# Kernel tuning notes

Measured on AMD Instinct MI355X. Metric: run time of the kernel, lower is better.

Reference implementation:

```python
import jax, jax.numpy as jnp
import numpy as np

DIM = 2048
HEADS = 16
DIM_HEAD = 128
DIM_INNER = HEADS * DIM_HEAD
BATCH = 2
SEQ = 2048
EPS = 1e-12  # F.normalize default eps


def l2norm(t, axis=-1):
    # matches F.normalize(t, dim=axis, p=2): t / max(||t||, eps)
    n = jnp.sqrt(jnp.sum(t * t, axis=axis, keepdims=True))
    return t / jnp.maximum(n, EPS)


def setup_inputs() -> dict:
    key = jax.random.key(0)
    ks = jax.random.split(key, 5)
    x = jax.random.normal(ks[0], (BATCH, SEQ, DIM), dtype=jnp.float32)
    # NormLinear weights (torch Linear layout: [out, in]); parametrization
    # l2-normalizes rows (dim=-1) for q/k/v and columns (dim=0) for to_out.
    Wq = jax.random.normal(ks[1], (DIM_INNER, DIM), dtype=jnp.float32) / np.sqrt(DIM)
    Wk = jax.random.normal(ks[2], (DIM_INNER, DIM), dtype=jnp.float32) / np.sqrt(DIM)
    Wv = jax.random.normal(ks[3], (DIM_INNER, DIM), dtype=jnp.float32) / np.sqrt(DIM)
    Wout = jax.random.normal(ks[4], (DIM, DIM_INNER), dtype=jnp.float32) / np.sqrt(DIM_INNER)
    # Scale(dim_inner, init=1.0, scale=dim**-1): param = ones * dim**-1,
    # forward_scale = init/scale = dim, so qk_scale() starts at 1.0
    qk_scale = jnp.ones((DIM_INNER,), dtype=jnp.float32) / DIM
    return {"x": x, "Wq": Wq, "Wk": Wk, "Wv": Wv, "Wout": Wout, "qk_scale": qk_scale}


def reference(x, Wq, Wk, Wv, Wout, qk_scale):
    b, n, _ = x.shape
    # NormLinear: x @ l2norm(W, rows).T  (scale = groups**-1 = 1)
    q = jnp.einsum('bnd,ed->bne', x, l2norm(Wq, axis=-1))
    k = jnp.einsum('bnd,ed->bne', x, l2norm(Wk, axis=-1))
    v = jnp.einsum('bnd,ed->bne', x, l2norm(Wv, axis=-1))
    # split heads: b n (h d) -> b h n d
    split = lambda t: t.reshape(b, n, HEADS, DIM_HEAD).transpose(0, 2, 1, 3)
    q, k, v = split(q), split(k), split(v)
    # per-head l2norm of q and k over head dim
    q = l2norm(q, axis=-1)
    k = l2norm(k, axis=-1)
    # learned qk scale: (h d) -> h 1 d, effective = param * forward_scale(=DIM)
    q = q * (qk_scale * DIM).reshape(HEADS, 1, DIM_HEAD)
    # causal SDPA with scale = sqrt(dim_head) (unit-norm q,k in nGPT)
    attn_scale = DIM_HEAD ** 0.5
    scores = jnp.einsum('bhid,bhjd->bhij', q, k) * attn_scale
    causal = jnp.tril(jnp.ones((n, n), dtype=bool))
    scores = jnp.where(causal, scores, jnp.finfo(scores.dtype).min)
    attn = jax.nn.softmax(scores, axis=-1)
    out = jnp.einsum('bhij,bhjd->bhid', attn, v)
    # merge heads: b h n d -> b n (h d)
    out = out.transpose(0, 2, 1, 3).reshape(b, n, DIM_INNER)
    # to_out: NormLinear with norm over dim=0 of weight [DIM, DIM_INNER]
    out = jnp.einsum('bne,de->bnd', out, l2norm(Wout, axis=0))
    return out
```

## Files before the change

kernel.cpp:

```cpp
#include <hip/hip_runtime.h>


typedef __bf16 bf16x8 __attribute__((ext_vector_type(8)));
typedef float f32x4 __attribute__((ext_vector_type(4)));

__device__ __forceinline__ unsigned short f2bf(float f) {
  unsigned int u = __float_as_uint(f);
  u = u + 0x7FFFu + ((u >> 16) & 1u);
  return (unsigned short)(u >> 16);
}

__device__ __forceinline__ void async16(const void* g, void* l) {
  __builtin_amdgcn_global_load_lds(
      (const __attribute__((address_space(1))) unsigned int*)g,
      (__attribute__((address_space(3))) unsigned int*)l, 16, 0, 0);
}

#define QFOLD (2048.0f * 11.313708498984761f * 1.4426950408889634f)


__global__ __launch_bounds__(256) void prep_w_rows(
    const float* __restrict__ Wq, const float* __restrict__ Wk,
    const float* __restrict__ Wv, ushort* __restrict__ oq,
    ushort* __restrict__ ok_, ushort* __restrict__ ov) {
  const int row = blockIdx.x;
  const float* W = (blockIdx.y == 0) ? Wq : (blockIdx.y == 1) ? Wk : Wv;
  ushort* O = (blockIdx.y == 0) ? oq : (blockIdx.y == 1) ? ok_ : ov;
  const int t = threadIdx.x;
  const float4* Wr = (const float4*)(W + (size_t)row * 2048);
  float4 v0 = Wr[t];
  float4 v1 = Wr[t + 256];
  float ss = v0.x * v0.x + v0.y * v0.y + v0.z * v0.z + v0.w * v0.w +
             v1.x * v1.x + v1.y * v1.y + v1.z * v1.z + v1.w * v1.w;
  ss += __shfl_xor(ss, 1);  ss += __shfl_xor(ss, 2);
  ss += __shfl_xor(ss, 4);  ss += __shfl_xor(ss, 8);
  ss += __shfl_xor(ss, 16); ss += __shfl_xor(ss, 32);
  __shared__ float red[4];
  if ((t & 63) == 0) red[t >> 6] = ss;
  __syncthreads();
  float tot = red[0] + red[1] + red[2] + red[3];
  float sc = 1.0f / fmaxf(sqrtf(tot), 1e-12f);
  ushort4 o0, o1;
  o0.x = f2bf(v0.x * sc); o0.y = f2bf(v0.y * sc);
  o0.z = f2bf(v0.z * sc); o0.w = f2bf(v0.w * sc);
  o1.x = f2bf(v1.x * sc); o1.y = f2bf(v1.y * sc);
  o1.z = f2bf(v1.z * sc); o1.w = f2bf(v1.w * sc);
  *(ushort4*)(O + (size_t)row * 2048 + t * 4) = o0;
  *(ushort4*)(O + (size_t)row * 2048 + 1024 + t * 4) = o1;
}

__global__ __launch_bounds__(256) void wout_colss(const float* __restrict__ W,
                                                  float* __restrict__ colss) {
  const int e = blockIdx.x * 256 + threadIdx.x;
  const int d0 = blockIdx.y * 128;
  float ss = 0.f;
  #pragma unroll 8
  for (int i = 0; i < 128; ++i) {
    float v = W[(size_t)(d0 + i) * 2048 + e];
    ss += v * v;
  }
  atomicAdd(colss + e, ss);
}

__global__ __launch_bounds__(256) void wout_norm(const float* __restrict__ W,
                                                 const float* __restrict__ colss,
                                                 ushort* __restrict__ O) {
  const int idx = (blockIdx.x * 256 + threadIdx.x) * 4;
  float4 v = *(const float4*)(W + idx);
  float4 c = *(const float4*)(colss + (idx & 2047));
  ushort4 o;
  o.x = f2bf(v.x / fmaxf(sqrtf(c.x), 1e-12f));
  o.y = f2bf(v.y / fmaxf(sqrtf(c.y), 1e-12f));
  o.z = f2bf(v.z / fmaxf(sqrtf(c.z), 1e-12f));
  o.w = f2bf(v.w / fmaxf(sqrtf(c.w), 1e-12f));
  *(ushort4*)(O + idx) = o;
}

__global__ __launch_bounds__(256) void convert_x(const float* __restrict__ X,
                                                 ushort* __restrict__ O) {
  const int idx = (blockIdx.x * 256 + threadIdx.x) * 4;
  float4 v = *(const float4*)(X + idx);
  ushort4 o;
  o.x = f2bf(v.x); o.y = f2bf(v.y); o.z = f2bf(v.z); o.w = f2bf(v.w);
  *(ushort4*)(O + idx) = o;
}

__global__ __launch_bounds__(64) void qk_mhead(const float* __restrict__ qks,
                                               float* __restrict__ mh) {
  const int h = blockIdx.x, l = threadIdx.x;
  float m = fmaxf(fabsf(qks[h * 128 + l]), fabsf(qks[h * 128 + 64 + l]));
  m = fmaxf(m, __shfl_xor(m, 1));  m = fmaxf(m, __shfl_xor(m, 2));
  m = fmaxf(m, __shfl_xor(m, 4));  m = fmaxf(m, __shfl_xor(m, 8));
  m = fmaxf(m, __shfl_xor(m, 16)); m = fmaxf(m, __shfl_xor(m, 32));
  if (l == 0) mh[h] = m * QFOLD;
}


#define LDSBUF 49152
#define ABYTES 32768

__device__ __forceinline__ void mainloop_256x128(
    const ushort* __restrict__ A, const ushort* __restrict__ Bw,
    int m0, int n0, char* lds, f32x4 acc[4][4], int t) {
  const int l = t & 63, w = t >> 6;
  const int wm = w & 3, wn = w >> 2;
  const int l15 = l & 15, l4 = l >> 4;

  const int lc = (t & 7) ^ ((t >> 3) & 7);
  const ushort* srcA = A + (size_t)m0 * 2048 + (t >> 3) * 2048 + lc * 8;
  const ushort* srcB = Bw + (size_t)n0 * 2048 + (t >> 3) * 2048 + lc * 8;
  char* dstA = lds + t * 16;
  char* dstB = lds + ABYTES + t * 16;

  const int rdA = (wm * 64 + l15) * 128;
  const int rdB = ABYTES + (wn * 64 + l15) * 128;
  const int cb0 = ((l4 ^ (l15 & 7)) * 16);
  const int cb1 = (((4 + l4) ^ (l15 & 7)) * 16);

  auto stageA = [&](int s, int k0, int o) {
    async16(srcA + (size_t)o * 131072 + k0, dstA + s * LDSBUF + o * 8192);
  };
  auto stageB = [&](int s, int k0, int o) {
    async16(srcB + (size_t)o * 131072 + k0, dstB + s * LDSBUF + o * 8192);
  };

  #pragma unroll
  for (int i = 0; i < 4; ++i)
    #pragma unroll
    for (int j = 0; j < 4; ++j) acc[i][j] = (f32x4){0.f, 0.f, 0.f, 0.f};

  stageA(0, 0, 0); stageA(0, 0, 1); stageA(0, 0, 2); stageA(0, 0, 3);
  stageB(0, 0, 0); stageB(0, 0, 1);
  stageA(1, 64, 0); stageA(1, 64, 1); stageA(1, 64, 2); stageA(1, 64, 3);
  stageB(1, 64, 0); stageB(1, 64, 1);
  asm volatile("s_waitcnt vmcnt(6)" ::: "memory");
  __builtin_amdgcn_s_barrier();

  auto tile = [&](int s, int s2, int k2, bool pf) {
    const char* Ab = lds + s * LDSBUF;
    bf16x8 af[4][2], bg[4][2];
    #pragma unroll
    for (int fm = 0; fm < 4; ++fm) {
      af[fm][0] = *(const bf16x8*)(Ab + rdA + fm * 2048 + cb0);
      af[fm][1] = *(const bf16x8*)(Ab + rdA + fm * 2048 + cb1);
    }
    #pragma unroll
    for (int fn = 0; fn < 2; ++fn) {
      bg[fn][0] = *(const bf16x8*)(Ab + rdB + fn * 2048 + cb0);
      bg[fn][1] = *(const bf16x8*)(Ab + rdB + fn * 2048 + cb1);
    }
    if (pf) { stageA(s2, k2, 0); stageA(s2, k2, 1); stageA(s2, k2, 2); }
    __builtin_amdgcn_s_setprio(1);
    #pragma unroll
    for (int ks = 0; ks < 2; ++ks)
      #pragma unroll
      for (int fm = 0; fm < 4; ++fm)
        #pragma unroll
        for (int fn = 0; fn < 2; ++fn)
          acc[fm][fn] = __builtin_amdgcn_mfma_f32_16x16x32_bf16(
              af[fm][ks], bg[fn][ks], acc[fm][fn], 0, 0, 0);
    __builtin_amdgcn_s_setprio(0);
    #pragma unroll
    for (int fn = 2; fn < 4; ++fn) {
      bg[fn][0] = *(const bf16x8*)(Ab + rdB + fn * 2048 + cb0);
      bg[fn][1] = *(const bf16x8*)(Ab + rdB + fn * 2048 + cb1);
    }
    if (pf) { stageA(s2, k2, 3); stageB(s2, k2, 0); stageB(s2, k2, 1); }
    __builtin_amdgcn_s_setprio(1);
    #pragma unroll
    for (int ks = 0; ks < 2; ++ks)
      #pragma unroll
      for (int fm = 0; fm < 4; ++fm)
        #pragma unroll
        for (int fn = 2; fn < 4; ++fn)
          acc[fm][fn] = __builtin_amdgcn_mfma_f32_16x16x32_bf16(
              af[fm][ks], bg[fn][ks], acc[fm][fn], 0, 0, 0);
    __builtin_amdgcn_s_setprio(0);
  };

  #pragma unroll 1
  for (int kt = 0; kt < 30; kt += 3) {
    tile(0, 2, (kt + 2) * 64, true);
    asm volatile("s_waitcnt vmcnt(6)" ::: "memory");
    __builtin_amdgcn_s_barrier();
    tile(1, 0, (kt + 3) * 64, true);
    asm volatile("s_waitcnt vmcnt(6)" ::: "memory");
    __builtin_amdgcn_s_barrier();
    tile(2, 1, (kt + 4) * 64, true);
    asm volatile("s_waitcnt vmcnt(6)" ::: "memory");
    __builtin_amdgcn_s_barrier();
  }
  tile(0, 0, 0, false);
  asm volatile("s_waitcnt vmcnt(0)" ::: "memory");
  __builtin_amdgcn_s_barrier();
  tile(1, 0, 0, false);
}

__global__ __launch_bounds__(512, 2) void gemm_qkv(
    const ushort* __restrict__ X, const ushort* __restrict__ Wq,
    const ushort* __restrict__ Wk, const ushort* __restrict__ Wv,
    const float* __restrict__ qks, ushort* __restrict__ qn,
    ushort* __restrict__ kn, ushort* __restrict__ vt) {
  __shared__ __align__(16) char lds[3 * LDSBUF];
  __shared__ float partials[2][256];
  const int z = blockIdx.z;
  const ushort* Bw = (z == 0) ? Wq : (z == 1) ? Wk : Wv;
  const int n0 = blockIdx.x * 128;
  const int m0 = blockIdx.y * 256;
  const int t = threadIdx.x;
  const int l = t & 63, w = t >> 6;
  const int wm = w & 3, wn = w >> 2;
  const int l15 = l & 15, l4 = l >> 4;

  f32x4 acc[4][4];
  mainloop_256x128(X, Bw, m0, n0, lds, acc, t);

  const int h = blockIdx.x;
  if (z == 2) {
    const int bb = m0 >> 11, nb = m0 & 2047;
    #pragma unroll
    for (int fm = 0; fm < 4; ++fm) {
      int nn = nb + wm * 64 + fm * 16 + l4 * 4;
      #pragma unroll
      for (int fn = 0; fn < 4; ++fn) {
        int d = wn * 64 + fn * 16 + l15;
        ushort4 p;
        p.x = f2bf(acc[fm][fn][0]); p.y = f2bf(acc[fm][fn][1]);
        p.z = f2bf(acc[fm][fn][2]); p.w = f2bf(acc[fm][fn][3]);
        *(ushort4*)(vt + (size_t)((bb * 16 + h) * 128 + d) * 2048 + nn) = p;
      }
    }
  } else {
    #pragma unroll
    for (int fm = 0; fm < 4; ++fm)
      #pragma unroll
      for (int r = 0; r < 4; ++r) {
        float s = 0.f;
        #pragma unroll
        for (int fn = 0; fn < 4; ++fn) {
          float v = acc[fm][fn][r];
          s += v * v;
        }
        s += __shfl_xor(s, 1); s += __shfl_xor(s, 2);
        s += __shfl_xor(s, 4); s += __shfl_xor(s, 8);
        if (l15 == 0) partials[wn][wm * 64 + fm * 16 + l4 * 4 + r] = s;
      }
    __syncthreads();
    float cs[4];
    #pragma unroll
    for (int fn = 0; fn < 4; ++fn)
      cs[fn] = (z == 0) ? qks[n0 + wn * 64 + fn * 16 + l15] * QFOLD : 1.0f;
    ushort* O = (z == 0) ? qn : kn;
    #pragma unroll
    for (int fm = 0; fm < 4; ++fm)
      #pragma unroll
      for (int r = 0; r < 4; ++r) {
        int i = wm * 64 + fm * 16 + l4 * 4 + r;
        float tot = partials[0][i] + partials[1][i];
        float sc = 1.0f / fmaxf(sqrtf(tot), 1e-12f);
        #pragma unroll
        for (int fn = 0; fn < 4; ++fn)
          O[(size_t)(m0 + i) * 2048 + n0 + wn * 64 + fn * 16 + l15] =
              f2bf(acc[fm][fn][r] * sc * cs[fn]);
      }
  }
}

__global__ __launch_bounds__(256, 3) void attn_kernel(
    const ushort* __restrict__ qn, const ushort* __restrict__ kn,
    const ushort* __restrict__ vt, const float* __restrict__ mhead,
    ushort* __restrict__ ao) {
  const int hb = blockIdx.x;
  const int b = hb >> 4, h = hb & 15;
  const int qt = 31 - blockIdx.y;
  const int i0 = qt * 64;
  const int t = threadIdx.x, w = t >> 6, l = t & 63;
  const int l15 = l & 15, l4 = l >> 4;

  __shared__ __align__(16) ushort Ks[64 * 136];
  __shared__ __align__(16) ushort Vts[128 * 72];
  __shared__ __align__(16) ushort Ps[64 * 72];

  bf16x8 qf[4];
  #pragma unroll
  for (int ks = 0; ks < 4; ++ks)
    qf[ks] = *(const bf16x8*)(qn +
        (size_t)(b * 2048 + i0 + w * 16 + l15) * 2048 +
        h * 128 + ks * 32 + l4 * 8);

  f32x4 Oa[8];
  #pragma unroll
  for (int fd = 0; fd < 8; ++fd) Oa[fd] = (f32x4){0.f, 0.f, 0.f, 0.f};
  f32x4 Ol = (f32x4){0.f, 0.f, 0.f, 0.f};

  const float mh = mhead[h];
  const __bf16 one = (__bf16)1.0f;
  const bf16x8 ones = {one, one, one, one, one, one, one, one};

  const ushort* kbase = kn + (size_t)(b * 2048) * 2048 + h * 128;
  const ushort* vbase = vt + (size_t)((b * 16 + h) * 128) * 2048;

  for (int jt = 0; jt <= qt; ++jt) {
    const int j0 = jt * 64;
    __syncthreads();
    #pragma unroll
    for (int pass = 0; pass < 5; ++pass) {
      int c = pass * 256 + t;
      if (c < 1088) {
        int r = c / 17, dc = c - r * 17;
        int dcc = (dc == 16) ? 0 : dc;
        async16(kbase + (size_t)(j0 + r) * 2048 + dcc * 8, (char*)Ks + c * 16);
      }
    }
    #pragma unroll
    for (int pass = 0; pass < 5; ++pass) {
      int c = pass * 256 + t;
      if (c < 1152) {
        int r = c / 9, jc = c - r * 9;
        int jcc = (jc == 8) ? 0 : jc;
        async16(vbase + (size_t)r * 2048 + j0 + jcc * 8, (char*)Vts + c * 16);
      }
    }
    __syncthreads();

    f32x4 Sa[4];
    #pragma unroll
    for (int fj = 0; fj < 4; ++fj) {
      f32x4 s0 = (f32x4){0.f, 0.f, 0.f, 0.f};
      #pragma unroll
      for (int ks = 0; ks < 4; ++ks) {
        bf16x8 kf = *(const bf16x8*)&Ks[(fj * 16 + l15) * 136 + ks * 32 + l4 * 8];
        s0 = __builtin_amdgcn_mfma_f32_16x16x32_bf16(qf[ks], kf, s0, 0, 0, 0);
      }
      Sa[fj] = s0;
    }

    if (jt == qt) {
      #pragma unroll
      for (int fj = 0; fj < 4; ++fj)
        #pragma unroll
        for (int r = 0; r < 4; ++r) {
          int jg = fj * 16 + l15;
          int ig = w * 16 + l4 * 4 + r;
          if (jg > ig) Sa[fj][r] = -1e30f;
        }
    }

    #pragma unroll
    for (int fj = 0; fj < 4; ++fj)
      #pragma unroll
      for (int r = 0; r < 4; ++r)
        Ps[(w * 16 + l4 * 4 + r) * 72 + fj * 16 + l15] =
            f2bf(__builtin_exp2f(Sa[fj][r] - mh));

    #pragma unroll
    for (int ks = 0; ks < 2; ++ks) {
      bf16x8 p0 = *(const bf16x8*)&Ps[(w * 16 + l15) * 72 + ks * 32 + l4 * 8];
      Ol = __builtin_amdgcn_mfma_f32_16x16x32_bf16(p0, ones, Ol, 0, 0, 0);
      #pragma unroll
      for (int fd = 0; fd < 8; ++fd) {
        bf16x8 vf = *(const bf16x8*)&Vts[(fd * 16 + l15) * 72 + ks * 32 + l4 * 8];
        Oa[fd] = __builtin_amdgcn_mfma_f32_16x16x32_bf16(p0, vf, Oa[fd], 0, 0, 0);
      }
    }
  }

  #pragma unroll
  for (int r = 0; r < 4; ++r) {
    float inv = 1.0f / Ol[r];
    int ig = i0 + w * 16 + l4 * 4 + r;
    #pragma unroll
    for (int fd = 0; fd < 8; ++fd)
      ao[(size_t)(b * 2048 + ig) * 2048 + h * 128 + fd * 16 + l15] =
          f2bf(Oa[fd][r] * inv);
  }
}

__global__ __launch_bounds__(512, 2) void gemm_out(
    const ushort* __restrict__ A, const ushort* __restrict__ Bw,
    float* __restrict__ C) {
  __shared__ __align__(16) char lds[3 * LDSBUF];
  const int n0 = blockIdx.x * 128;
  const int m0 = blockIdx.y * 256;
  const int t = threadIdx.x;
  const int l = t & 63, w = t >> 6;
  const int wm = w & 3, wn = w >> 2;
  const int l15 = l & 15, l4 = l >> 4;

  f32x4 acc[4][4];
  mainloop_256x128(A, Bw, m0, n0, lds, acc, t);

  #pragma unroll
  for (int fm = 0; fm < 4; ++fm)
    #pragma unroll
    for (int fn = 0; fn < 4; ++fn)
      #pragma unroll
      for (int r = 0; r < 4; ++r)
        C[(size_t)(m0 + wm * 64 + fm * 16 + l4 * 4 + r) * 2048 +
          n0 + wn * 64 + fn * 16 + l15] = acc[fm][fn][r];
}

extern "C" void kernel_launch(void* const* d_in, const int* in_sizes, int n_in,
                              void* d_out, int out_size, void* d_ws, size_t ws_size,
                              hipStream_t stream) {
  (void)in_sizes; (void)n_in; (void)out_size; (void)ws_size;
  const float* x    = (const float*)d_in[0];
  const float* Wq   = (const float*)d_in[1];
  const float* Wk   = (const float*)d_in[2];
  const float* Wv   = (const float*)d_in[3];
  const float* Wout = (const float*)d_in[4];
  const float* qks  = (const float*)d_in[5];
  char* ws = (char*)d_ws;

  ushort* wqn  = (ushort*)(ws + 0);
  ushort* wkn  = (ushort*)(ws + 8388608);
  ushort* wvn  = (ushort*)(ws + 16777216);
  ushort* wotn = (ushort*)(ws + 25165824);
  ushort* xbf  = (ushort*)(ws + 33554432);
  ushort* qn   = (ushort*)(ws + 50331648);
  ushort* kn   = (ushort*)(ws + 67108864);
  ushort* vt   = (ushort*)(ws + 83886080);
  ushort* ao   = (ushort*)(ws + 100663296);
  float* colss = (float*)(ws + 117440512);
  float* mh    = (float*)(ws + 117448704);
  float* out   = (float*)d_out;

  hipMemsetAsync(colss, 0, 2048 * sizeof(float), stream);
  prep_w_rows<<<dim3(2048, 3), 256, 0, stream>>>(Wq, Wk, Wv, wqn, wkn, wvn);
  wout_colss<<<dim3(8, 16), 256, 0, stream>>>(Wout, colss);
  wout_norm<<<4096, 256, 0, stream>>>(Wout, colss, wotn);
  convert_x<<<8192, 256, 0, stream>>>(x, xbf);
  qk_mhead<<<16, 64, 0, stream>>>(qks, mh);
  gemm_qkv<<<dim3(16, 16, 3), 512, 0, stream>>>(xbf, wqn, wkn, wvn, qks, qn, kn, vt);
  attn_kernel<<<dim3(32, 32), 256, 0, stream>>>(qn, kn, vt, mh, ao);
  gemm_out<<<dim3(16, 16), 512, 0, stream>>>(ao, wotn, out);
}
```

Measured before the change: 376.5 us.

## Use 256x256 tiles with 4-stage K=32 ring pipeline for QKV GEMM

The QKV projection GEMM moves from 256x128 tiles with a 3-stage K=64 buffer to 256x256 tiles with a 4-deep ring of K=32 stages. Each of the 8 waves now holds 8x4 accumulator fragments. This halves the grid and doubles arithmetic intensity per loaded byte, so global and LDS traffic per FLOP drop. The epilogues are adjusted so each head pair reduces its row norms and V is transposed per head. The costs are more accumulator registers per thread, 128KB of LDS, and fewer blocks (384), which may limit occupancy and load balance at 2 blocks per CU.

```diff
diff --git a/kernel.cpp b/kernel.cpp
--- a/kernel.cpp
+++ b/kernel.cpp
@@ -96,104 +96,92 @@
 }
 
 
-#define LDSBUF 49152
-#define ABYTES 32768
-
-__device__ __forceinline__ void mainloop_256x128(
+__device__ __forceinline__ void mainloop_256sq(
     const ushort* __restrict__ A, const ushort* __restrict__ Bw,
-    int m0, int n0, char* lds, f32x4 acc[4][4], int t) {
+    int m0, int n0, char* ring, f32x4 acc[8][4], int t) {
   const int l = t & 63, w = t >> 6;
-  const int wm = w & 3, wn = w >> 2;
+  const int wm = w & 1, wn = w >> 1;
   const int l15 = l & 15, l4 = l >> 4;
 
-  const int lc = (t & 7) ^ ((t >> 3) & 7);
-  const ushort* srcA = A + (size_t)m0 * 2048 + (t >> 3) * 2048 + lc * 8;
-  const ushort* srcB = Bw + (size_t)n0 * 2048 + (t >> 3) * 2048 + lc * 8;
-  char* dstA = lds + t * 16;
-  char* dstB = lds + ABYTES + t * 16;
-
-  const int rdA = (wm * 64 + l15) * 128;
-  const int rdB = ABYTES + (wn * 64 + l15) * 128;
-  const int cb0 = ((l4 ^ (l15 & 7)) * 16);
-  const int cb1 = (((4 + l4) ^ (l15 & 7)) * 16);
-
-  auto stageA = [&](int s, int k0, int o) {
-    async16(srcA + (size_t)o * 131072 + k0, dstA + s * LDSBUF + o * 8192);
+  const int srow = t >> 2;
+  const int lc = (t & 3) ^ (srow & 3);
+  const ushort* sA = A + (size_t)(m0 + srow) * 2048 + lc * 8;
+  const ushort* sB = Bw + (size_t)(n0 + srow) * 2048 + lc * 8;
+  char* dA = ring + t * 16;
+  char* dB = ring + 16384 + t * 16;
+
+  const int swz = (l4 ^ (l15 & 3)) * 16;
+  const int raA = (wm * 128 + l15) * 64 + swz;
+  const int raB = 16384 + (wn * 64 + l15) * 64 + swz;
+
+  auto stA = [&](int buf, int kt) {
+    async16(sA + kt * 32,          dA + buf * 32768);
+    async16(sA + kt * 32 + 262144, dA + buf * 32768 + 8192);
   };
-  auto stageB = [&](int s, int k0, int o) {
-    async16(srcB + (size_t)o * 131072 + k0, dstB + s * LDSBUF + o * 8192);
+  auto stB = [&](int buf, int kt) {
+    async16(sB + kt * 32,          dB + buf * 32768);
+    async16(sB + kt * 32 + 262144, dB + buf * 32768 + 8192);
   };
 
   #pragma unroll
-  for (int i = 0; i < 4; ++i)
+  for (int i = 0; i < 8; ++i)
     #pragma unroll
     for (int j = 0; j < 4; ++j) acc[i][j] = (f32x4){0.f, 0.f, 0.f, 0.f};
 
-  stageA(0, 0, 0); stageA(0, 0, 1); stageA(0, 0, 2); stageA(0, 0, 3);
-  stageB(0, 0, 0); stageB(0, 0, 1);
-  stageA(1, 64, 0); stageA(1, 64, 1); stageA(1, 64, 2); stageA(1, 64, 3);
-  stageB(1, 64, 0); stageB(1, 64, 1);
-  asm volatile("s_waitcnt vmcnt(6)" ::: "memory");
-  __builtin_amdgcn_s_barrier();
-
-  auto tile = [&](int s, int s2, int k2, bool pf) {
-    const char* Ab = lds + s * LDSBUF;
-    bf16x8 af[4][2], bg[4][2];
-    #pragma unroll
-    for (int fm = 0; fm < 4; ++fm) {
-      af[fm][0] = *(const bf16x8*)(Ab + rdA + fm * 2048 + cb0);
-      af[fm][1] = *(const bf16x8*)(Ab + rdA + fm * 2048 + cb1);
-    }
-    #pragma unroll
-    for (int fn = 0; fn < 2; ++fn) {
-      bg[fn][0] = *(const bf16x8*)(Ab + rdB + fn * 2048 + cb0);
-      bg[fn][1] = *(const bf16x8*)(Ab + rdB + fn * 2048 + cb1);
-    }
-    if (pf) { stageA(s2, k2, 0); stageA(s2, k2, 1); stageA(s2, k2, 2); }
+  auto tile = [&](int buf, bool pf, int pbuf, int pkt) {
+    const char* base = ring + buf * 32768;
+    bf16x8 a[4], b[4];
+    #pragma unroll
+    for (int fm = 0; fm < 4; ++fm)
+      a[fm] = *(const bf16x8*)(base + raA + fm * 1024);
+    #pragma unroll
+    for (int fn = 0; fn < 4; ++fn)
+      b[fn] = *(const bf16x8*)(base + raB + fn * 1024);
+    if (pf) stA(pbuf, pkt);
+    __builtin_amdgcn_s_barrier();
     __builtin_amdgcn_s_setprio(1);
     #pragma unroll
-    for (int ks = 0; ks < 2; ++ks)
-      #pragma unroll
-      for (int fm = 0; fm < 4; ++fm)
-        #pragma unroll
-        for (int fn = 0; fn < 2; ++fn)
-          acc[fm][fn] = __builtin_amdgcn_mfma_f32_16x16x32_bf16(
-              af[fm][ks], bg[fn][ks], acc[fm][fn], 0, 0, 0);
+    for (int fm = 0; fm < 4; ++fm)
+      #pragma unroll
+      for (int fn = 0; fn < 4; ++fn)
+        acc[fm][fn] = __builtin_amdgcn_mfma_f32_16x16x32_bf16(
+            a[fm], b[fn], acc[fm][fn], 0, 0, 0);
     __builtin_amdgcn_s_setprio(0);
-    #pragma unroll
-    for (int fn = 2; fn < 4; ++fn) {
-      bg[fn][0] = *(const bf16x8*)(Ab + rdB + fn * 2048 + cb0);
-      bg[fn][1] = *(const bf16x8*)(Ab + rdB + fn * 2048 + cb1);
-    }
-    if (pf) { stageA(s2, k2, 3); stageB(s2, k2, 0); stageB(s2, k2, 1); }
+    __builtin_amdgcn_s_barrier();
+    #pragma unroll
+    for (int fm = 0; fm < 4; ++fm)
+      a[fm] = *(const bf16x8*)(base + raA + (4 + fm) * 1024);
+    if (pf) stB(pbuf, pkt);
+    __builtin_amdgcn_s_barrier();
     __builtin_amdgcn_s_setprio(1);
     #pragma unroll
-    for (int ks = 0; ks < 2; ++ks)
-      #pragma unroll
-      for (int fm = 0; fm < 4; ++fm)
-        #pragma unroll
-        for (int fn = 2; fn < 4; ++fn)
-          acc[fm][fn] = __builtin_amdgcn_mfma_f32_16x16x32_bf16(
-              af[fm][ks], bg[fn][ks], acc[fm][fn], 0, 0, 0);
+    for (int fm = 0; fm < 4; ++fm)
+      #pragma unroll
+      for (int fn = 0; fn < 4; ++fn)
+        acc[4 + fm][fn] = __builtin_amdgcn_mfma_f32_16x16x32_bf16(
+            a[fm], b[fn], acc[4 + fm][fn], 0, 0, 0);
     __builtin_amdgcn_s_setprio(0);
   };
 
+  stA(0, 0); stB(0, 0);
+  stA(1, 1); stB(1, 1);
+  stA(2, 2); stB(2, 2);
+  asm volatile("s_waitcnt vmcnt(8)" ::: "memory");
+  __builtin_amdgcn_s_barrier();
+
   #pragma unroll 1
-  for (int kt = 0; kt < 30; kt += 3) {
-    tile(0, 2, (kt + 2) * 64, true);
-    asm volatile("s_waitcnt vmcnt(6)" ::: "memory");
-    __builtin_amdgcn_s_barrier();
-    tile(1, 0, (kt + 3) * 64, true);
-    asm volatile("s_waitcnt vmcnt(6)" ::: "memory");
-    __builtin_amdgcn_s_barrier();
-    tile(2, 1, (kt + 4) * 64, true);
-    asm volatile("s_waitcnt vmcnt(6)" ::: "memory");
+  for (int kt = 0; kt < 61; ++kt) {
+    tile(kt & 3, true, (kt + 3) & 3, kt + 3);
+    asm volatile("s_waitcnt vmcnt(8)" ::: "memory");
     __builtin_amdgcn_s_barrier();
   }
-  tile(0, 0, 0, false);
+  tile(61 & 3, false, 0, 0);
+  asm volatile("s_waitcnt vmcnt(4)" ::: "memory");
+  __builtin_amdgcn_s_barrier();
+  tile(62 & 3, false, 0, 0);
   asm volatile("s_waitcnt vmcnt(0)" ::: "memory");
   __builtin_amdgcn_s_barrier();
-  tile(1, 0, 0, false);
+  tile(63 & 3, false, 0, 0);
 }
 
 __global__ __launch_bounds__(512, 2) void gemm_qkv(
@@ -201,29 +189,30 @@
     const ushort* __restrict__ Wk, const ushort* __restrict__ Wv,
     const float* __restrict__ qks, ushort* __restrict__ qn,
     ushort* __restrict__ kn, ushort* __restrict__ vt) {
-  __shared__ __align__(16) char lds[3 * LDSBUF];
-  __shared__ float partials[2][256];
+  __shared__ __align__(16) char ring[4 * 32768];
+  __shared__ float partials[4][256];
   const int z = blockIdx.z;
   const ushort* Bw = (z == 0) ? Wq : (z == 1) ? Wk : Wv;
-  const int n0 = blockIdx.x * 128;
+  const int n0 = blockIdx.x * 256;
   const int m0 = blockIdx.y * 256;
   const int t = threadIdx.x;
   const int l = t & 63, w = t >> 6;
-  const int wm = w & 3, wn = w >> 2;
+  const int wm = w & 1, wn = w >> 1;
   const int l15 = l & 15, l4 = l >> 4;
 
-  f32x4 acc[4][4];
-  mainloop_256x128(X, Bw, m0, n0, lds, acc, t);
-
-  const int h = blockIdx.x;
+  f32x4 acc[8][4];
+  mainloop_256sq(X, Bw, m0, n0, ring, acc, t);
+
   if (z == 2) {
-    const int bb = m0 >> 11, nb = m0 & 2047;
-    #pragma unroll
-    for (int fm = 0; fm < 4; ++fm) {
-      int nn = nb + wm * 64 + fm * 16 + l4 * 4;
+    #pragma unroll
+    for (int fm = 0; fm < 8; ++fm) {
+      int mrow = m0 + wm * 128 + fm * 16 + l4 * 4;
+      int bb = mrow >> 11;
+      int nn = mrow & 2047;
       #pragma unroll
       for (int fn = 0; fn < 4; ++fn) {
-        int d = wn * 64 + fn * 16 + l15;
+        int col = n0 + wn * 64 + fn * 16 + l15;
+        int h = col >> 7, d = col & 127;
         ushort4 p;
         p.x = f2bf(acc[fm][fn][0]); p.y = f2bf(acc[fm][fn][1]);
         p.z = f2bf(acc[fm][fn][2]); p.w = f2bf(acc[fm][fn][3]);
@@ -232,7 +221,7 @@
     }
   } else {
     #pragma unroll
-    for (int fm = 0; fm < 4; ++fm)
+    for (int fm = 0; fm < 8; ++fm)
       #pragma unroll
       for (int r = 0; r < 4; ++r) {
         float s = 0.f;
@@ -243,7 +232,7 @@
         }
         s += __shfl_xor(s, 1); s += __shfl_xor(s, 2);
         s += __shfl_xor(s, 4); s += __shfl_xor(s, 8);
-        if (l15 == 0) partials[wn][wm * 64 + fm * 16 + l4 * 4 + r] = s;
+        if (l15 == 0) partials[wn][wm * 128 + fm * 16 + l4 * 4 + r] = s;
       }
     __syncthreads();
     float cs[4];
@@ -251,12 +240,13 @@
     for (int fn = 0; fn < 4; ++fn)
       cs[fn] = (z == 0) ? qks[n0 + wn * 64 + fn * 16 + l15] * QFOLD : 1.0f;
     ushort* O = (z == 0) ? qn : kn;
-    #pragma unroll
-    for (int fm = 0; fm < 4; ++fm)
+    const int hp = (wn >> 1) * 2;
+    #pragma unroll
+    for (int fm = 0; fm < 8; ++fm)
       #pragma unroll
       for (int r = 0; r < 4; ++r) {
-        int i = wm * 64 + fm * 16 + l4 * 4 + r;
-        float tot = partials[0][i] + partials[1][i];
+        int i = wm * 128 + fm * 16 + l4 * 4 + r;
+        float tot = partials[hp][i] + partials[hp + 1][i];
         float sc = 1.0f / fmaxf(sqrtf(tot), 1e-12f);
         #pragma unroll
         for (int fn = 0; fn < 4; ++fn)
@@ -264,6 +254,107 @@
               f2bf(acc[fm][fn][r] * sc * cs[fn]);
       }
   }
+}
+
+
+#define LDSBUF 49152
+#define ABYTES 32768
+
+__device__ __forceinline__ void mainloop_256x128(
+    const ushort* __restrict__ A, const ushort* __restrict__ Bw,
+    int m0, int n0, char* lds, f32x4 acc[4][4], int t) {
+  const int l = t & 63, w = t >> 6;
+  const int wm = w & 3, wn = w >> 2;
+  const int l15 = l & 15, l4 = l >> 4;
+
+  const int lc = (t & 7) ^ ((t >> 3) & 7);
+  const ushort* srcA = A + (size_t)m0 * 2048 + (t >> 3) * 2048 + lc * 8;
+  const ushort* srcB = Bw + (size_t)n0 * 2048 + (t >> 3) * 2048 + lc * 8;
+  char* dstA = lds + t * 16;
+  char* dstB = lds + ABYTES + t * 16;
+
+  const int rdA = (wm * 64 + l15) * 128;
+  const int rdB = ABYTES + (wn * 64 + l15) * 128;
+  const int cb0 = ((l4 ^ (l15 & 7)) * 16);
+  const int cb1 = (((4 + l4) ^ (l15 & 7)) * 16);
+
+  auto stageA = [&](int s, int k0, int o) {
+    async16(srcA + (size_t)o * 131072 + k0, dstA + s * LDSBUF + o * 8192);
+  };
+  auto stageB = [&](int s, int k0, int o) {
+    async16(srcB + (size_t)o * 131072 + k0, dstB + s * LDSBUF + o * 8192);
+  };
+
+  #pragma unroll
+  for (int i = 0; i < 4; ++i)
+    #pragma unroll
+    for (int j = 0; j < 4; ++j) acc[i][j] = (f32x4){0.f, 0.f, 0.f, 0.f};
+
+  stageA(0, 0, 0); stageA(0, 0, 1); stageA(0, 0, 2); stageA(0, 0, 3);
+  stageB(0, 0, 0); stageB(0, 0, 1);
+  stageA(1, 64, 0); stageA(1, 64, 1); stageA(1, 64, 2); stageA(1, 64, 3);
+  stageB(1, 64, 0); stageB(1, 64, 1);
+  asm volatile("s_waitcnt vmcnt(6)" ::: "memory");
+  __builtin_amdgcn_s_barrier();
+
+  auto tile = [&](int s, int s2, int k2, bool pf) {
+    const char* Ab = lds + s * LDSBUF;
+    bf16x8 af[4][2], bg[4][2];
+    #pragma unroll
+    for (int fm = 0; fm < 4; ++fm) {
+      af[fm][0] = *(const bf16x8*)(Ab + rdA + fm * 2048 + cb0);
+      af[fm][1] = *(const bf16x8*)(Ab + rdA + fm * 2048 + cb1);
+    }
+    #pragma unroll
+    for (int fn = 0; fn < 2; ++fn) {
+      bg[fn][0] = *(const bf16x8*)(Ab + rdB + fn * 2048 + cb0);
+      bg[fn][1] = *(const bf16x8*)(Ab + rdB + fn * 2048 + cb1);
+    }
+    if (pf) { stageA(s2, k2, 0); stageA(s2, k2, 1); stageA(s2, k2, 2); }
+    __builtin_amdgcn_s_setprio(1);
+    #pragma unroll
+    for (int ks = 0; ks < 2; ++ks)
+      #pragma unroll
+      for (int fm = 0; fm < 4; ++fm)
+        #pragma unroll
+        for (int fn = 0; fn < 2; ++fn)
+          acc[fm][fn] = __builtin_amdgcn_mfma_f32_16x16x32_bf16(
+              af[fm][ks], bg[fn][ks], acc[fm][fn], 0, 0, 0);
+    __builtin_amdgcn_s_setprio(0);
+    #pragma unroll
+    for (int fn = 2; fn < 4; ++fn) {
+      bg[fn][0] = *(const bf16x8*)(Ab + rdB + fn * 2048 + cb0);
+      bg[fn][1] = *(const bf16x8*)(Ab + rdB + fn * 2048 + cb1);
+    }
+    if (pf) { stageA(s2, k2, 3); stageB(s2, k2, 0); stageB(s2, k2, 1); }
+    __builtin_amdgcn_s_setprio(1);
+    #pragma unroll
+    for (int ks = 0; ks < 2; ++ks)
+      #pragma unroll
+      for (int fm = 0; fm < 4; ++fm)
+        #pragma unroll
+        for (int fn = 2; fn < 4; ++fn)
+          acc[fm][fn] = __builtin_amdgcn_mfma_f32_16x16x32_bf16(
+              af[fm][ks], bg[fn][ks], acc[fm][fn], 0, 0, 0);
+    __builtin_amdgcn_s_setprio(0);
+  };
+
+  #pragma unroll 1
+  for (int kt = 0; kt < 30; kt += 3) {
+    tile(0, 2, (kt + 2) * 64, true);
+    asm volatile("s_waitcnt vmcnt(6)" ::: "memory");
+    __builtin_amdgcn_s_barrier();
+    tile(1, 0, (kt + 3) * 64, true);
+    asm volatile("s_waitcnt vmcnt(6)" ::: "memory");
+    __builtin_amdgcn_s_barrier();
+    tile(2, 1, (kt + 4) * 64, true);
+    asm volatile("s_waitcnt vmcnt(6)" ::: "memory");
+    __builtin_amdgcn_s_barrier();
+  }
+  tile(0, 0, 0, false);
+  asm volatile("s_waitcnt vmcnt(0)" ::: "memory");
+  __builtin_amdgcn_s_barrier();
+  tile(1, 0, 0, false);
 }
 
 __global__ __launch_bounds__(256, 3) void attn_kernel(
@@ -431,7 +522,7 @@
   wout_norm<<<4096, 256, 0, stream>>>(Wout, colss, wotn);
   convert_x<<<8192, 256, 0, stream>>>(x, xbf);
   qk_mhead<<<16, 64, 0, stream>>>(qks, mh);
-  gemm_qkv<<<dim3(16, 16, 3), 512, 0, stream>>>(xbf, wqn, wkn, wvn, qks, qn, kn, vt);
+  gemm_qkv<<<dim3(8, 16, 3), 512, 0, stream>>>(xbf, wqn, wkn, wvn, qks, qn, kn, vt);
   attn_kernel<<<dim3(32, 32), 256, 0, stream>>>(qn, kn, vt, mh, ao);
   gemm_out<<<dim3(16, 16), 512, 0, stream>>>(ao, wotn, out);
 }
```

New measurement: 410.2 us. 1.09x slower.

## Enlarge attention query tile with swizzled LDS and simplify the QKV GEMM

Applied to the files above, without the earlier changes.

Attention blocks now process 128 query rows instead of 64, so each block reuses the K/V tiles loaded into LDS across twice as many rows. The grid is halved, the block order is remapped for causal balance, and padded LDS rows are replaced with XOR-swizzled layouts for K, V^T and P. The QKV projection moves from the triple-buffered, pipelined 256x128 mainloop to a simple single-buffered 128x128 loop with 256 threads and higher occupancy. That may lose latency hiding on the largest GEMM, and the attention kernel now has higher register pressure at occupancy 2.

```diff
diff --git a/kernel.cpp b/kernel.cpp
--- a/kernel.cpp
+++ b/kernel.cpp
@@ -95,6 +95,131 @@
   if (l == 0) mh[h] = m * QFOLD;
 }
 
+__device__ __forceinline__ void gemm_mainloop(
+    const ushort* __restrict__ A, const ushort* __restrict__ Bw,
+    int m0, int n0, ushort* As, ushort* Bs, f32x4 acc[4][4],
+    int t, int l, int wm, int wn) {
+  const int l15 = l & 15, l4 = l >> 4;
+  const ushort* abase = A + (size_t)m0 * 2048;
+  const ushort* bbase = Bw + (size_t)n0 * 2048;
+  for (int kt = 0; kt < 32; ++kt) {
+    const int k0 = kt * 64;
+    __syncthreads();
+    #pragma unroll
+    for (int p = 0; p < 9; ++p) {
+      int c = p * 256 + t;
+      const ushort* src = abase;
+      char* dst = (char*)As;
+      int cc = c;
+      if (c >= 1152) { cc = c - 1152; src = bbase; dst = (char*)Bs; }
+      int r = cc / 9, dc = cc - r * 9;
+      int dcc = (dc == 8) ? 0 : dc;
+      async16(src + (size_t)r * 2048 + k0 + dcc * 8, dst + cc * 16);
+    }
+    __syncthreads();
+    #pragma unroll
+    for (int ks = 0; ks < 2; ++ks) {
+      bf16x8 af[4], bg[4];
+      #pragma unroll
+      for (int f = 0; f < 4; ++f)
+        af[f] = *(const bf16x8*)&As[(wm * 64 + f * 16 + l15) * 72 + ks * 32 + l4 * 8];
+      #pragma unroll
+      for (int f = 0; f < 4; ++f)
+        bg[f] = *(const bf16x8*)&Bs[(wn * 64 + f * 16 + l15) * 72 + ks * 32 + l4 * 8];
+      #pragma unroll
+      for (int fm = 0; fm < 4; ++fm)
+        #pragma unroll
+        for (int fn = 0; fn < 4; ++fn)
+          acc[fm][fn] = __builtin_amdgcn_mfma_f32_16x16x32_bf16(
+              af[fm], bg[fn], acc[fm][fn], 0, 0, 0);
+    }
+  }
+}
+
+__global__ __launch_bounds__(256, 4) void gemm_qkv(
+    const ushort* __restrict__ X, const ushort* __restrict__ Wq,
+    const ushort* __restrict__ Wk, const ushort* __restrict__ Wv,
+    const float* __restrict__ qks, ushort* __restrict__ qn,
+    ushort* __restrict__ kn, ushort* __restrict__ vt) {
+  const int z = blockIdx.z;
+  const ushort* Bw = (z == 0) ? Wq : (z == 1) ? Wk : Wv;
+  const int n0 = blockIdx.x * 128;
+  const int m0 = blockIdx.y * 128;
+  __shared__ __align__(16) ushort As[128 * 72];
+  __shared__ __align__(16) ushort Bs[128 * 72];
+  __shared__ float partials[2][128];
+  const int t = threadIdx.x, w = t >> 6, l = t & 63;
+  const int wm = w & 1, wn = w >> 1;
+  const int l15 = l & 15, l4 = l >> 4;
+
+  f32x4 acc[4][4];
+  #pragma unroll
+  for (int i = 0; i < 4; ++i)
+    #pragma unroll
+    for (int j = 0; j < 4; ++j) acc[i][j] = (f32x4){0.f, 0.f, 0.f, 0.f};
+
+  gemm_mainloop(X, Bw, m0, n0, As, Bs, acc, t, l, wm, wn);
+
+  const int h = n0 >> 7;
+  if (z == 2) {
+    #pragma unroll
+    for (int fm = 0; fm < 4; ++fm) {
+      int mrow = m0 + wm * 64 + fm * 16 + l4 * 4;
+      int bb = mrow >> 11;
+      int nn = mrow & 2047;
+      #pragma unroll
+      for (int fn = 0; fn < 4; ++fn) {
+        int d = wn * 64 + fn * 16 + l15;
+        ushort4 p;
+        p.x = f2bf(acc[fm][fn][0]); p.y = f2bf(acc[fm][fn][1]);
+        p.z = f2bf(acc[fm][fn][2]); p.w = f2bf(acc[fm][fn][3]);
+        *(ushort4*)(vt + (size_t)((bb * 16 + h) * 128 + d) * 2048 + nn) = p;
+      }
+    }
+  } else {
+    float rs[4][4];
+    #pragma unroll
+    for (int fm = 0; fm < 4; ++fm)
+      #pragma unroll
+      for (int r = 0; r < 4; ++r) {
+        float s = 0.f;
+        #pragma unroll
+        for (int fn = 0; fn < 4; ++fn) {
+          float v = acc[fm][fn][r];
+          s += v * v;
+        }
+        s += __shfl_xor(s, 1); s += __shfl_xor(s, 2);
+        s += __shfl_xor(s, 4); s += __shfl_xor(s, 8);
+        rs[fm][r] = s;
+      }
+    if (l15 == 0) {
+      #pragma unroll
+      for (int fm = 0; fm < 4; ++fm)
+        #pragma unroll
+        for (int r = 0; r < 4; ++r)
+          partials[wn][wm * 64 + fm * 16 + l4 * 4 + r] = rs[fm][r];
+    }
+    __syncthreads();
+    float cs[4];
+    #pragma unroll
+    for (int fn = 0; fn < 4; ++fn)
+      cs[fn] = (z == 0) ? qks[n0 + wn * 64 + fn * 16 + l15] * QFOLD : 1.0f;
+    ushort* O = (z == 0) ? qn : kn;
+    #pragma unroll
+    for (int fm = 0; fm < 4; ++fm)
+      #pragma unroll
+      for (int r = 0; r < 4; ++r) {
+        int i = wm * 64 + fm * 16 + l4 * 4 + r;
+        float tot = partials[0][i] + partials[1][i];
+        float sc = 1.0f / fmaxf(sqrtf(tot), 1e-12f);
+        #pragma unroll
+        for (int fn = 0; fn < 4; ++fn)
+          O[(size_t)(m0 + i) * 2048 + n0 + wn * 64 + fn * 16 + l15] =
+              f2bf(acc[fm][fn][r] * sc * cs[fn]);
+      }
+  }
+}
+
 
 #define LDSBUF 49152
 #define ABYTES 32768
@@ -196,102 +321,39 @@
   tile(1, 0, 0, false);
 }
 
-__global__ __launch_bounds__(512, 2) void gemm_qkv(
-    const ushort* __restrict__ X, const ushort* __restrict__ Wq,
-    const ushort* __restrict__ Wk, const ushort* __restrict__ Wv,
-    const float* __restrict__ qks, ushort* __restrict__ qn,
-    ushort* __restrict__ kn, ushort* __restrict__ vt) {
-  __shared__ __align__(16) char lds[3 * LDSBUF];
-  __shared__ float partials[2][256];
-  const int z = blockIdx.z;
-  const ushort* Bw = (z == 0) ? Wq : (z == 1) ? Wk : Wv;
-  const int n0 = blockIdx.x * 128;
-  const int m0 = blockIdx.y * 256;
-  const int t = threadIdx.x;
-  const int l = t & 63, w = t >> 6;
-  const int wm = w & 3, wn = w >> 2;
-  const int l15 = l & 15, l4 = l >> 4;
-
-  f32x4 acc[4][4];
-  mainloop_256x128(X, Bw, m0, n0, lds, acc, t);
-
-  const int h = blockIdx.x;
-  if (z == 2) {
-    const int bb = m0 >> 11, nb = m0 & 2047;
-    #pragma unroll
-    for (int fm = 0; fm < 4; ++fm) {
-      int nn = nb + wm * 64 + fm * 16 + l4 * 4;
-      #pragma unroll
-      for (int fn = 0; fn < 4; ++fn) {
-        int d = wn * 64 + fn * 16 + l15;
-        ushort4 p;
-        p.x = f2bf(acc[fm][fn][0]); p.y = f2bf(acc[fm][fn][1]);
-        p.z = f2bf(acc[fm][fn][2]); p.w = f2bf(acc[fm][fn][3]);
-        *(ushort4*)(vt + (size_t)((bb * 16 + h) * 128 + d) * 2048 + nn) = p;
-      }
-    }
-  } else {
-    #pragma unroll
-    for (int fm = 0; fm < 4; ++fm)
-      #pragma unroll
-      for (int r = 0; r < 4; ++r) {
-        float s = 0.f;
-        #pragma unroll
-        for (int fn = 0; fn < 4; ++fn) {
-          float v = acc[fm][fn][r];
-          s += v * v;
-        }
-        s += __shfl_xor(s, 1); s += __shfl_xor(s, 2);
-        s += __shfl_xor(s, 4); s += __shfl_xor(s, 8);
-        if (l15 == 0) partials[wn][wm * 64 + fm * 16 + l4 * 4 + r] = s;
-      }
-    __syncthreads();
-    float cs[4];
-    #pragma unroll
-    for (int fn = 0; fn < 4; ++fn)
-      cs[fn] = (z == 0) ? qks[n0 + wn * 64 + fn * 16 + l15] * QFOLD : 1.0f;
-    ushort* O = (z == 0) ? qn : kn;
-    #pragma unroll
-    for (int fm = 0; fm < 4; ++fm)
-      #pragma unroll
-      for (int r = 0; r < 4; ++r) {
-        int i = wm * 64 + fm * 16 + l4 * 4 + r;
-        float tot = partials[0][i] + partials[1][i];
-        float sc = 1.0f / fmaxf(sqrtf(tot), 1e-12f);
-        #pragma unroll
-        for (int fn = 0; fn < 4; ++fn)
-          O[(size_t)(m0 + i) * 2048 + n0 + wn * 64 + fn * 16 + l15] =
-              f2bf(acc[fm][fn][r] * sc * cs[fn]);
-      }
-  }
-}
-
-__global__ __launch_bounds__(256, 3) void attn_kernel(
+__global__ __launch_bounds__(256, 2) void attn_kernel(
     const ushort* __restrict__ qn, const ushort* __restrict__ kn,
     const ushort* __restrict__ vt, const float* __restrict__ mhead,
     ushort* __restrict__ ao) {
   const int hb = blockIdx.x;
   const int b = hb >> 4, h = hb & 15;
-  const int qt = 31 - blockIdx.y;
-  const int i0 = qt * 64;
+  const int y = blockIdx.y;
+  const int qt = (y < 8) ? y : 23 - y;
+  const int i0 = qt * 128;
   const int t = threadIdx.x, w = t >> 6, l = t & 63;
   const int l15 = l & 15, l4 = l >> 4;
 
-  __shared__ __align__(16) ushort Ks[64 * 136];
-  __shared__ __align__(16) ushort Vts[128 * 72];
-  __shared__ __align__(16) ushort Ps[64 * 72];
-
-  bf16x8 qf[4];
+  __shared__ __align__(16) ushort Ks[64 * 128];
+  __shared__ __align__(16) ushort Vts[128 * 64];
+  __shared__ __align__(16) ushort Ps[128 * 64];
+
+  bf16x8 qf[2][4];
   #pragma unroll
-  for (int ks = 0; ks < 4; ++ks)
-    qf[ks] = *(const bf16x8*)(qn +
-        (size_t)(b * 2048 + i0 + w * 16 + l15) * 2048 +
-        h * 128 + ks * 32 + l4 * 8);
-
-  f32x4 Oa[8];
+  for (int fmq = 0; fmq < 2; ++fmq)
+    #pragma unroll
+    for (int ks = 0; ks < 4; ++ks)
+      qf[fmq][ks] = *(const bf16x8*)(qn +
+          (size_t)(b * 2048 + i0 + w * 32 + fmq * 16 + l15) * 2048 +
+          h * 128 + ks * 32 + l4 * 8);
+
+  f32x4 Oa[2][8];
   #pragma unroll
-  for (int fd = 0; fd < 8; ++fd) Oa[fd] = (f32x4){0.f, 0.f, 0.f, 0.f};
-  f32x4 Ol = (f32x4){0.f, 0.f, 0.f, 0.f};
+  for (int fmq = 0; fmq < 2; ++fmq)
+    #pragma unroll
+    for (int fd = 0; fd < 8; ++fd) Oa[fmq][fd] = (f32x4){0.f, 0.f, 0.f, 0.f};
+  f32x4 Ol[2];
+  Ol[0] = (f32x4){0.f, 0.f, 0.f, 0.f};
+  Ol[1] = (f32x4){0.f, 0.f, 0.f, 0.f};
 
   const float mh = mhead[h];
   const __bf16 one = (__bf16)1.0f;
@@ -300,80 +362,103 @@
   const ushort* kbase = kn + (size_t)(b * 2048) * 2048 + h * 128;
   const ushort* vbase = vt + (size_t)((b * 16 + h) * 128) * 2048;
 
-  for (int jt = 0; jt <= qt; ++jt) {
+  const int jtmax = 2 * qt + 1;
+  for (int jt = 0; jt <= jtmax; ++jt) {
     const int j0 = jt * 64;
     __syncthreads();
     #pragma unroll
-    for (int pass = 0; pass < 5; ++pass) {
-      int c = pass * 256 + t;
-      if (c < 1088) {
-        int r = c / 17, dc = c - r * 17;
-        int dcc = (dc == 16) ? 0 : dc;
-        async16(kbase + (size_t)(j0 + r) * 2048 + dcc * 8, (char*)Ks + c * 16);
+    for (int i = 0; i < 4; ++i) {
+      int g = i * 256 + t;
+      int r = g >> 4, pc = g & 15;
+      async16(kbase + (size_t)(j0 + r) * 2048 + (pc ^ (r & 7)) * 8,
+              (char*)Ks + g * 16);
+    }
+    #pragma unroll
+    for (int i = 0; i < 4; ++i) {
+      int g = i * 256 + t;
+      int r = g >> 3, pc = g & 7;
+      async16(vbase + (size_t)r * 2048 + j0 + (pc ^ (r & 7)) * 8,
+              (char*)Vts + g * 16);
+    }
+    __syncthreads();
+
+    f32x4 Sa[2][4];
+    #pragma unroll
+    for (int fj = 0; fj < 4; ++fj) {
+      bf16x8 kf[4];
+      #pragma unroll
+      for (int ks = 0; ks < 4; ++ks)
+        kf[ks] = *(const bf16x8*)&Ks[(fj * 16 + l15) * 128 +
+                                     ((ks * 4 + l4) ^ (l15 & 7)) * 8];
+      #pragma unroll
+      for (int fmq = 0; fmq < 2; ++fmq) {
+        f32x4 s0 = (f32x4){0.f, 0.f, 0.f, 0.f};
+        #pragma unroll
+        for (int ks = 0; ks < 4; ++ks)
+          s0 = __builtin_amdgcn_mfma_f32_16x16x32_bf16(qf[fmq][ks], kf[ks],
+                                                       s0, 0, 0, 0);
+        Sa[fmq][fj] = s0;
       }
     }
-    #pragma unroll
-    for (int pass = 0; pass < 5; ++pass) {
-      int c = pass * 256 + t;
-      if (c < 1152) {
-        int r = c / 9, jc = c - r * 9;
-        int jcc = (jc == 8) ? 0 : jc;
-        async16(vbase + (size_t)r * 2048 + j0 + jcc * 8, (char*)Vts + c * 16);
+
+    if (jt >= 2 * qt) {
+      #pragma unroll
+      for (int fmq = 0; fmq < 2; ++fmq)
+        #pragma unroll
+        for (int fj = 0; fj < 4; ++fj)
+          #pragma unroll
+          for (int r = 0; r < 4; ++r) {
+            int jg = j0 + fj * 16 + l15;
+            int ig = i0 + w * 32 + fmq * 16 + l4 * 4 + r;
+            if (jg > ig) Sa[fmq][fj][r] = -1e30f;
+          }
+    }
+
+    #pragma unroll
+    for (int fmq = 0; fmq < 2; ++fmq)
+      #pragma unroll
+      for (int fj = 0; fj < 4; ++fj)
+        #pragma unroll
+        for (int r = 0; r < 4; ++r) {
+          int qr = w * 32 + fmq * 16 + l4 * 4 + r;
+          Ps[qr * 64 + ((fj * 16 + l15) ^ ((qr & 7) << 3))] =
+              f2bf(__builtin_exp2f(Sa[fmq][fj][r] - mh));
+        }
+
+    #pragma unroll
+    for (int ks = 0; ks < 2; ++ks) {
+      bf16x8 p0[2];
+      #pragma unroll
+      for (int fmq = 0; fmq < 2; ++fmq) {
+        int qr = w * 32 + fmq * 16 + l15;
+        p0[fmq] = *(const bf16x8*)&Ps[qr * 64 +
+                                      ((ks * 4 + l4) ^ (l15 & 7)) * 8];
+        Ol[fmq] = __builtin_amdgcn_mfma_f32_16x16x32_bf16(p0[fmq], ones,
+                                                          Ol[fmq], 0, 0, 0);
       }
-    }
-    __syncthreads();
-
-    f32x4 Sa[4];
-    #pragma unroll
-    for (int fj = 0; fj < 4; ++fj) {
-      f32x4 s0 = (f32x4){0.f, 0.f, 0.f, 0.f};
-      #pragma unroll
-      for (int ks = 0; ks < 4; ++ks) {
-        bf16x8 kf = *(const bf16x8*)&Ks[(fj * 16 + l15) * 136 + ks * 32 + l4 * 8];
-        s0 = __builtin_amdgcn_mfma_f32_16x16x32_bf16(qf[ks], kf, s0, 0, 0, 0);
+      #pragma unroll
+      for (int fd = 0; fd < 8; ++fd) {
+        bf16x8 vf = *(const bf16x8*)&Vts[(fd * 16 + l15) * 64 +
+                                         ((ks * 4 + l4) ^ (l15 & 7)) * 8];
+        #pragma unroll
+        for (int fmq = 0; fmq < 2; ++fmq)
+          Oa[fmq][fd] = __builtin_amdgcn_mfma_f32_16x16x32_bf16(
+              p0[fmq], vf, Oa[fmq][fd], 0, 0, 0);
       }
-      Sa[fj] = s0;
-    }
-
-    if (jt == qt) {
-      #pragma unroll
-      for (int fj = 0; fj < 4; ++fj)
-        #pragma unroll
-        for (int r = 0; r < 4; ++r) {
-          int jg = fj * 16 + l15;
-          int ig = w * 16 + l4 * 4 + r;
-          if (jg > ig) Sa[fj][r] = -1e30f;
-        }
-    }
-
-    #pragma unroll
-    for (int fj = 0; fj < 4; ++fj)
-      #pragma unroll
-      for (int r = 0; r < 4; ++r)
-        Ps[(w * 16 + l4 * 4 + r) * 72 + fj * 16 + l15] =
-            f2bf(__builtin_exp2f(Sa[fj][r] - mh));
-
-    #pragma unroll
-    for (int ks = 0; ks < 2; ++ks) {
-      bf16x8 p0 = *(const bf16x8*)&Ps[(w * 16 + l15) * 72 + ks * 32 + l4 * 8];
-      Ol = __builtin_amdgcn_mfma_f32_16x16x32_bf16(p0, ones, Ol, 0, 0, 0);
-      #pragma unroll
-      for (int fd = 0; fd < 8; ++fd) {
-        bf16x8 vf = *(const bf16x8*)&Vts[(fd * 16 + l15) * 72 + ks * 32 + l4 * 8];
-        Oa[fd] = __builtin_amdgcn_mfma_f32_16x16x32_bf16(p0, vf, Oa[fd], 0, 0, 0);
-      }
     }
   }
 
   #pragma unroll
-  for (int r = 0; r < 4; ++r) {
-    float inv = 1.0f / Ol[r];
-    int ig = i0 + w * 16 + l4 * 4 + r;
-    #pragma unroll
-    for (int fd = 0; fd < 8; ++fd)
-      ao[(size_t)(b * 2048 + ig) * 2048 + h * 128 + fd * 16 + l15] =
-          f2bf(Oa[fd][r] * inv);
-  }
+  for (int fmq = 0; fmq < 2; ++fmq)
+    #pragma unroll
+    for (int r = 0; r < 4; ++r) {
+      float inv = 1.0f / Ol[fmq][r];
+      int ig = i0 + w * 32 + fmq * 16 + l4 * 4 + r;
+      #pragma unroll
+      for (int fd = 0; fd < 8; ++fd)
+        ao[(size_t)(b * 2048 + ig) * 2048 + h * 128 + fd * 16 + l15] =
+            f2bf(Oa[fmq][fd][r] * inv);
+    }
 }
 
 __global__ __launch_bounds__(512, 2) void gemm_out(
@@ -431,7 +516,7 @@
   wout_norm<<<4096, 256, 0, stream>>>(Wout, colss, wotn);
   convert_x<<<8192, 256, 0, stream>>>(x, xbf);
   qk_mhead<<<16, 64, 0, stream>>>(qks, mh);
-  gemm_qkv<<<dim3(16, 16, 3), 512, 0, stream>>>(xbf, wqn, wkn, wvn, qks, qn, kn, vt);
-  attn_kernel<<<dim3(32, 32), 256, 0, stream>>>(qn, kn, vt, mh, ao);
+  gemm_qkv<<<dim3(16, 32, 3), 256, 0, stream>>>(xbf, wqn, wkn, wvn, qks, qn, kn, vt);
+  attn_kernel<<<dim3(32, 16), 256, 0, stream>>>(qn, kn, vt, mh, ao);
   gemm_out<<<dim3(16, 16), 512, 0, stream>>>(ao, wotn, out);
 }
```

Result: slower. 384.0 us (+2.0%).
